# Optimization experiments

Measured on AMD Instinct MI355X. Metric: run time of the kernel, lower is better.

## Reference

```python
import jax, jax.numpy as jnp
import numpy as np

N_SRC, N_DST = 20000, 20000
N = N_SRC + N_DST            # homogeneous node count
E = 320000                   # bipartite edges
H, D, IN = 8, 16, 128        # heads, per-head dim, input dim
TEM = 0.7
NEG_SLOPE = 0.2              # DGL GATConv leaky_relu slope
E_NEG = E - int(round(E * 0.01))  # drop-edge keeps 316800 edges


def setup_inputs() -> dict:
    key = jax.random.key(0)
    ks = jax.random.split(key, 6)
    feat = jax.random.normal(ks[0], (N, IN), jnp.float32)
    edge_src = jax.random.randint(ks[1], (E,), 0, N_SRC, dtype=jnp.int32)
    edge_dst = jax.random.randint(ks[2], (E,), 0, N_DST, dtype=jnp.int32) + N_SRC
    rng = np.random.default_rng(0)
    neg_idx = jnp.asarray(np.sort(rng.permutation(E)[:E_NEG]).astype(np.int32))
    fc_w = jax.random.normal(ks[3], (IN, H * D), jnp.float32) / np.sqrt(IN).astype(np.float32)
    attn_l = jax.random.normal(ks[4], (H, D), jnp.float32) * 0.1
    attn_r = jax.random.normal(ks[5], (H, D), jnp.float32) * 0.1
    bias = jnp.zeros((H * D,), jnp.float32)
    prelu_a = jnp.full((1,), 0.25, jnp.float32)
    return dict(feat=feat, fc_w=fc_w, attn_l=attn_l, attn_r=attn_r, bias=bias,
                prelu_a=prelu_a, edge_src=edge_src, edge_dst=edge_dst, neg_idx=neg_idx)


def _gat(feat, fc_w, attn_l, attn_r, bias, prelu_a, src, dst):
    """DGL GATConv (attn_drop=0, bias=True, activation=PReLU) + self-loops, then head-mean."""
    loop = jnp.arange(N, dtype=src.dtype)
    src = jnp.concatenate([src, loop])
    dst = jnp.concatenate([dst, loop])
    z = (feat @ fc_w).reshape(N, H, D)                 # [N,H,D]
    el = jnp.sum(z * attn_l[None], axis=-1)            # [N,H]
    er = jnp.sum(z * attn_r[None], axis=-1)            # [N,H]
    e = el[src] + er[dst]                              # [E',H]
    e = jnp.where(e >= 0, e, NEG_SLOPE * e)            # leaky_relu
    # segment (edge) softmax over incoming edges of each dst node
    m = jax.ops.segment_max(e, dst, num_segments=N)
    w = jnp.exp(e - m[dst])
    denom = jax.ops.segment_sum(w, dst, num_segments=N)
    alpha = w / denom[dst]                             # [E',H]
    msg = alpha[:, :, None] * z[src]                   # [E',H,D]
    rst = jax.ops.segment_sum(msg, dst, num_segments=N)  # [N,H,D]
    rst = rst + bias.reshape(1, H, D)
    rst = jnp.where(rst >= 0, rst, prelu_a[0] * rst)   # PReLU (single param)
    return jnp.mean(rst, axis=1)                       # [N,D] head-mean


def reference(feat, fc_w, attn_l, attn_r, bias, prelu_a, edge_src, edge_dst, neg_idx):
    h = _gat(feat, fc_w, attn_l, attn_r, bias, prelu_a, edge_src, edge_dst)
    h_neg_full = _gat(feat, fc_w, attn_l, attn_r, bias, prelu_a,
                      edge_src[neg_idx], edge_dst[neg_idx])
    # predict-type (dst) nodes are ids [N_SRC, N)
    h_pos = h[N_SRC:]
    h_neg = h_neg_full[N_SRC:]
    eps = 1e-8
    num = jnp.sum(h_pos * h_neg, axis=-1)
    na = jnp.maximum(jnp.linalg.norm(h_pos, axis=-1), eps)
    nb = jnp.maximum(jnp.linalg.norm(h_neg, axis=-1), eps)
    cos = num / (na * nb)                              # F.cosine_similarity
    loss = jnp.log(jnp.sum(jnp.exp(cos / TEM)))
    return loss, h_pos
```

## Files before the change

kernel.cpp:

```cpp
#include <hip/hip_runtime.h>

#define NSRC 20000
#define NDST 20000
#define NTOT 40000
#define ETOT 320000
#define ENEG 316800
#define NH 8
#define ND 16
#define NHD 128
#define BSTRIDE 136

typedef __bf16 v8bf __attribute__((ext_vector_type(8)));
typedef float v4f __attribute__((ext_vector_type(4)));


__global__ __launch_bounds__(256) void k_front(const float* __restrict__ A,
                                               const float* __restrict__ B,
                                               const float* __restrict__ attn_l,
                                               const float* __restrict__ attn_r,
                                               const int* __restrict__ edge_dst,
                                               const int* __restrict__ neg_idx,
                                               unsigned short* __restrict__ z,
                                               float* __restrict__ el,
                                               float* __restrict__ er,
                                               int* __restrict__ count,
                                               unsigned char* __restrict__ flag) {
    const int tid = threadIdx.x;
    const int bid = blockIdx.x;
    if (bid >= 625) {
        int t0 = (bid - 625) * 256 + tid;
        for (int i = t0; i < ETOT; i += 32768)
            atomicAdd(&count[edge_dst[i] - NSRC], 1);
        for (int i = t0; i < ENEG; i += 32768) flag[neg_idx[i]] = 1;
        return;
    }
    __shared__ __bf16 Bs[128 * BSTRIDE];
    for (int i = tid; i < 4096; i += 256) {
        float4 v = ((const float4*)B)[i];
        int k = (i * 4) >> 7;
        int n = (i * 4) & 127;
        Bs[(n + 0) * BSTRIDE + k] = (__bf16)v.x;
        Bs[(n + 1) * BSTRIDE + k] = (__bf16)v.y;
        Bs[(n + 2) * BSTRIDE + k] = (__bf16)v.z;
        Bs[(n + 3) * BSTRIDE + k] = (__bf16)v.w;
    }
    __syncthreads();
    const int w = tid >> 6, lane = tid & 63;
    const int ml = lane & 15, q = lane >> 4;
    const int gm = bid * 64 + w * 16 + ml;
    v4f acc[8];
#pragma unroll
    for (int n = 0; n < 8; ++n) acc[n] = (v4f){0.f, 0.f, 0.f, 0.f};
#pragma unroll
    for (int ks = 0; ks < 4; ++ks) {
        const int k0 = ks * 32 + q * 8;
        float4 f0 = *(const float4*)(A + (size_t)gm * 128 + k0);
        float4 f1 = *(const float4*)(A + (size_t)gm * 128 + k0 + 4);
        v8bf av;
        av[0] = (__bf16)f0.x; av[1] = (__bf16)f0.y;
        av[2] = (__bf16)f0.z; av[3] = (__bf16)f0.w;
        av[4] = (__bf16)f1.x; av[5] = (__bf16)f1.y;
        av[6] = (__bf16)f1.z; av[7] = (__bf16)f1.w;
#pragma unroll
        for (int n = 0; n < 8; ++n) {
            v8bf bv = *(const v8bf*)(&Bs[(n * 16 + ml) * BSTRIDE + k0]);
            acc[n] = __builtin_amdgcn_mfma_f32_16x16x32_bf16(av, bv, acc[n], 0, 0, 0);
        }
    }
    const int rowbase = bid * 64 + w * 16 + q * 4;
#pragma unroll
    for (int n = 0; n < 8; ++n) {
        float alv = attn_l[n * 16 + ml];
        float arv = attn_r[n * 16 + ml];
#pragma unroll
        for (int r = 0; r < 4; ++r) {
            float v = acc[n][r];
            unsigned int u = __float_as_uint(v);
            unsigned int b = (u + 0x7fffu + ((u >> 16) & 1u)) >> 16;
            z[(size_t)(rowbase + r) * NHD + n * 16 + ml] = (unsigned short)b;
            float pl = v * alv, pr = v * arv;
#pragma unroll
            for (int s = 1; s <= 8; s <<= 1) {
                pl += __shfl_xor(pl, s, 64);
                pr += __shfl_xor(pr, s, 64);
            }
            if (ml == 0) {
                el[(rowbase + r) * NH + n] = pl;
                er[(rowbase + r) * NH + n] = pr;
            }
        }
    }
}

__global__ __launch_bounds__(1024) void k_scan(const int* __restrict__ count,
                                               int* __restrict__ rowstart) {
    __shared__ int wsum[16];
    const int tid = threadIdx.x;
    const int lane = tid & 63, w = tid >> 6;
    const int base = tid * 20;
    int c[20];
    int s = 0;
#pragma unroll
    for (int k = 0; k < 20; ++k) {
        int i = base + k;
        int v = (i < NDST) ? count[i] : 0;
        c[k] = s;
        s += v;
    }
    int v = s;
    for (int sh = 1; sh < 64; sh <<= 1) {
        int t = __shfl_up(v, sh, 64);
        if (lane >= sh) v += t;
    }
    if (lane == 63) wsum[w] = v;
    __syncthreads();
    int carry = 0;
    for (int ww = 0; ww < w; ++ww) carry += wsum[ww];
    int excl = carry + v - s;
#pragma unroll
    for (int k = 0; k < 20; ++k) {
        int i = base + k;
        if (i < NDST) rowstart[i] = excl + c[k];
    }
    if (tid == 1023) rowstart[NDST] = carry + v;
}

__global__ __launch_bounds__(256) void k_scatter(const int* __restrict__ edge_src,
                                                 const int* __restrict__ edge_dst,
                                                 const unsigned char* __restrict__ flag,
                                                 const int* __restrict__ rowstart,
                                                 int* __restrict__ cursor,
                                                 int* __restrict__ csr) {
    int i = blockIdx.x * 256 + threadIdx.x;
    if (i >= ETOT) return;
    int d = edge_dst[i] - NSRC;
    int pos = rowstart[d] + atomicAdd(&cursor[d], 1);
    int v = edge_src[i];
    if (flag[i]) v |= (int)0x80000000u;
    csr[pos] = v;
}

__global__ __launch_bounds__(256) void k_agg(const int* __restrict__ rowstart,
                                             const int* __restrict__ csr,
                                             const unsigned short* __restrict__ z,
                                             const float* __restrict__ el,
                                             const float* __restrict__ er,
                                             const float* __restrict__ bias,
                                             const float* __restrict__ prelu_a,
                                             float* __restrict__ out,
                                             float* __restrict__ expcos) {
    const int lane = threadIdx.x & 63;
    const int wid = threadIdx.x >> 6;
    const int d = (blockIdx.x << 2) + wid;

    const int g = NSRC + d;
    const int hl = lane >> 3;
    const int j8 = lane & 7;
    const float erd = er[g * NH + hl];
    const float aslope = prelu_a[0];
    const float NEGINF = -__builtin_inff();

    float mF = NEGINF, lF = 0.f, mN = NEGINF, lN = 0.f;
    float aF0 = 0.f, aF1 = 0.f, aN0 = 0.f, aN1 = 0.f;
    const int rs = rowstart[d];
    const int deg = rowstart[d + 1] - rs;

    for (int base = 0; base < deg; base += 16) {
        const int j0 = base + j8, j1 = base + 8 + j8;
        int ent0 = (j0 < deg) ? csr[rs + j0] : g;
        int ent1 = (j1 < deg) ? csr[rs + j1] : g;
        unsigned int zr[16];
#pragma unroll
        for (int jj = 0; jj < 16; ++jj) {
            int entry = __shfl((jj < 8) ? ent0 : ent1, jj & 7, 64);
            zr[jj] = *(const unsigned int*)(z + ((size_t)(entry & 0x7FFFFFFF) << 7) + 2 * lane);
        }
        float e0 = el[(size_t)(ent0 & 0x7FFFFFFF) * NH + hl] + erd;
        float e1 = el[(size_t)(ent1 & 0x7FFFFFFF) * NH + hl] + erd;
        e0 = (e0 >= 0.f) ? e0 : 0.2f * e0;
        e1 = (e1 >= 0.f) ? e1 : 0.2f * e1;
        float ev0 = (j0 < deg) ? e0 : NEGINF;
        float ev1 = (j1 < deg) ? e1 : NEGINF;
        const int fl0 = (j0 < deg) && (ent0 < 0);
        const int fl1 = (j1 < deg) && (ent1 < 0);
        float cmF = fmaxf(ev0, ev1);
        float cmN = fmaxf(fl0 ? ev0 : NEGINF, fl1 ? ev1 : NEGINF);
#pragma unroll
        for (int s = 1; s <= 4; s <<= 1) {
            cmF = fmaxf(cmF, __shfl_xor(cmF, s, 64));
            cmN = fmaxf(cmN, __shfl_xor(cmN, s, 64));
        }
        float nmF = fmaxf(mF, cmF);
        float scF = (nmF == mF) ? 1.f : __expf(mF - nmF);
        mF = nmF;
        float nmN = fmaxf(mN, cmN);
        float scN = (nmN == mN) ? 1.f : __expf(mN - nmN);
        mN = nmN;
        float wf0 = __expf(ev0 - mF);
        float wf1 = __expf(ev1 - mF);
        float wn0 = fl0 ? __expf(ev0 - mN) : 0.f;
        float wn1 = fl1 ? __expf(ev1 - mN) : 0.f;
        lF = lF * scF + wf0 + wf1;
        lN = lN * scN + wn0 + wn1;
        float w0 = fl0 ? -wf0 : wf0;
        float w1 = fl1 ? -wf1 : wf1;
        float sNh = __expf(mF - mN);
        aF0 *= scF; aF1 *= scF; aN0 *= scN; aN1 *= scN;
#pragma unroll
        for (int jj = 0; jj < 16; ++jj) {
            float v = __shfl((jj < 8) ? w0 : w1, (lane & 56) | (jj & 7), 64);
            float wf = fabsf(v);
            float wn = (v < 0.f) ? wf * sNh : 0.f;
            float zx = __uint_as_float(zr[jj] << 16);
            float zy = __uint_as_float(zr[jj] & 0xffff0000u);
            aF0 = fmaf(wf, zx, aF0);
            aF1 = fmaf(wf, zy, aF1);
            aN0 = fmaf(wn, zx, aN0);
            aN1 = fmaf(wn, zy, aN1);
        }
    }

    {
        float e = el[g * NH + hl] + erd;
        e = (e >= 0.f) ? e : 0.2f * e;
        float nmF = fmaxf(mF, e);
        float scF = (nmF == mF) ? 1.f : __expf(mF - nmF);
        lF *= scF; aF0 *= scF; aF1 *= scF; mF = nmF;
        float wf = __expf(e - mF);
        float nmN = fmaxf(mN, e);
        float scN = (nmN == mN) ? 1.f : __expf(mN - nmN);
        lN *= scN; aN0 *= scN; aN1 *= scN; mN = nmN;
        float wn = __expf(e - mN);
        if (j8 == 0) { lF += wf; lN += wn; }
        unsigned int zv = *(const unsigned int*)(z + ((size_t)g << 7) + 2 * lane);
        float zx = __uint_as_float(zv << 16);
        float zy = __uint_as_float(zv & 0xffff0000u);
        aF0 = fmaf(wf, zx, aF0);
        aF1 = fmaf(wf, zy, aF1);
        aN0 = fmaf(wn, zx, aN0);
        aN1 = fmaf(wn, zy, aN1);
    }

#pragma unroll
    for (int s = 1; s <= 4; s <<= 1) {
        lF += __shfl_xor(lF, s, 64);
        lN += __shfl_xor(lN, s, 64);
    }
    const int c0 = 2 * lane;
    float b0 = bias[c0], b1 = bias[c0 + 1];
    float rF0 = aF0 / lF + b0, rF1 = aF1 / lF + b1;
    float rN0 = aN0 / lN + b0, rN1 = aN1 / lN + b1;
    rF0 = (rF0 >= 0.f) ? rF0 : aslope * rF0;
    rF1 = (rF1 >= 0.f) ? rF1 : aslope * rF1;
    rN0 = (rN0 >= 0.f) ? rN0 : aslope * rN0;
    rN1 = (rN1 >= 0.f) ? rN1 : aslope * rN1;
#pragma unroll
    for (int s = 8; s <= 32; s <<= 1) {
        rF0 += __shfl_xor(rF0, s, 64);
        rF1 += __shfl_xor(rF1, s, 64);
        rN0 += __shfl_xor(rN0, s, 64);
        rN1 += __shfl_xor(rN1, s, 64);
    }
    float hF0 = rF0 * 0.125f, hF1 = rF1 * 0.125f;
    float hN0 = rN0 * 0.125f, hN1 = rN1 * 0.125f;
    if (lane < 8) {
        out[1 + d * ND + 2 * lane] = hF0;
        out[1 + d * ND + 2 * lane + 1] = hF1;
    }
    float num = hF0 * hN0 + hF1 * hN1;
    float na = hF0 * hF0 + hF1 * hF1;
    float nb = hN0 * hN0 + hN1 * hN1;
#pragma unroll
    for (int s = 1; s <= 4; s <<= 1) {
        num += __shfl_xor(num, s, 64);
        na += __shfl_xor(na, s, 64);
        nb += __shfl_xor(nb, s, 64);
    }
    if (lane == 0) {
        float cosv = num / (fmaxf(sqrtf(na), 1e-8f) * fmaxf(sqrtf(nb), 1e-8f));
        expcos[d] = __expf(cosv / 0.7f);
    }
}

__global__ __launch_bounds__(1024) void k_loss(const float* __restrict__ expcos,
                                               float* __restrict__ out) {
    __shared__ float sbuf[16];
    float s = 0.f;
    for (int i = threadIdx.x; i < NDST; i += 1024) s += expcos[i];
    for (int sh = 1; sh < 64; sh <<= 1) s += __shfl_xor(s, sh, 64);
    if ((threadIdx.x & 63) == 0) sbuf[threadIdx.x >> 6] = s;
    __syncthreads();
    if (threadIdx.x < 16) {
        float t = sbuf[threadIdx.x];
        for (int sh = 1; sh < 16; sh <<= 1) t += __shfl_xor(t, sh, 16);
        if (threadIdx.x == 0) out[0] = logf(t);
    }
}

extern "C" void kernel_launch(void* const* d_in, const int* in_sizes, int n_in,
                              void* d_out, int out_size, void* d_ws, size_t ws_size,
                              hipStream_t stream) {
    const float* feat = (const float*)d_in[0];
    const float* fc_w = (const float*)d_in[1];
    const float* attn_l = (const float*)d_in[2];
    const float* attn_r = (const float*)d_in[3];
    const float* bias = (const float*)d_in[4];
    const float* prelu_a = (const float*)d_in[5];
    const int* edge_src = (const int*)d_in[6];
    const int* edge_dst = (const int*)d_in[7];
    const int* neg_idx = (const int*)d_in[8];
    float* out = (float*)d_out;

    char* ws = (char*)d_ws;
    int* count = (int*)(ws + 0);
    int* cursor = (int*)(ws + 80000);
    unsigned char* flag = (unsigned char*)(ws + 160000);
    int* rowstart = (int*)(ws + 480000);
    int* csr = (int*)(ws + 560064);
    float* expcos = (float*)(ws + 1840064);
    unsigned short* z = (unsigned short*)(ws + 1920064);
    float* el = (float*)(ws + 12160064);
    float* er = (float*)(ws + 13440064);

    hipMemsetAsync(d_ws, 0, 480000, stream);
    k_front<<<753, 256, 0, stream>>>(feat, fc_w, attn_l, attn_r, edge_dst,
                                     neg_idx, z, el, er, count, flag);
    k_scan<<<1, 1024, 0, stream>>>(count, rowstart);
    k_scatter<<<(ETOT + 255) / 256, 256, 0, stream>>>(edge_src, edge_dst, flag,
                                                      rowstart, cursor, csr);
    k_agg<<<NDST / 4, 256, 0, stream>>>(rowstart, csr, z, el, er, bias, prelu_a,
                                        out, expcos);
    k_loss<<<1, 1024, 0, stream>>>(expcos, out);
}
```

Baseline: 178.7 us.

## Replace count/scan CSR with fixed-capacity per-node buckets and share softmax max

```diff
diff --git a/kernel.cpp b/kernel.cpp
--- a/kernel.cpp
+++ b/kernel.cpp
@@ -8,6 +8,7 @@
 #define NH 8
 #define ND 16
 #define NHD 128
+#define BCAP 64
 #define BSTRIDE 136
 
 typedef __bf16 v8bf __attribute__((ext_vector_type(8)));
@@ -18,19 +19,15 @@
                                                const float* __restrict__ B,
                                                const float* __restrict__ attn_l,
                                                const float* __restrict__ attn_r,
-                                               const int* __restrict__ edge_dst,
                                                const int* __restrict__ neg_idx,
                                                unsigned short* __restrict__ z,
                                                float* __restrict__ el,
                                                float* __restrict__ er,
-                                               int* __restrict__ count,
                                                unsigned char* __restrict__ flag) {
     const int tid = threadIdx.x;
     const int bid = blockIdx.x;
     if (bid >= 625) {
         int t0 = (bid - 625) * 256 + tid;
-        for (int i = t0; i < ETOT; i += 32768)
-            atomicAdd(&count[edge_dst[i] - NSRC], 1);
         for (int i = t0; i < ENEG; i += 32768) flag[neg_idx[i]] = 1;
         return;
     }
@@ -92,55 +89,21 @@
     }
 }
 
-__global__ __launch_bounds__(1024) void k_scan(const int* __restrict__ count,
-                                               int* __restrict__ rowstart) {
-    __shared__ int wsum[16];
-    const int tid = threadIdx.x;
-    const int lane = tid & 63, w = tid >> 6;
-    const int base = tid * 20;
-    int c[20];
-    int s = 0;
-#pragma unroll
-    for (int k = 0; k < 20; ++k) {
-        int i = base + k;
-        int v = (i < NDST) ? count[i] : 0;
-        c[k] = s;
-        s += v;
-    }
-    int v = s;
-    for (int sh = 1; sh < 64; sh <<= 1) {
-        int t = __shfl_up(v, sh, 64);
-        if (lane >= sh) v += t;
-    }
-    if (lane == 63) wsum[w] = v;
-    __syncthreads();
-    int carry = 0;
-    for (int ww = 0; ww < w; ++ww) carry += wsum[ww];
-    int excl = carry + v - s;
-#pragma unroll
-    for (int k = 0; k < 20; ++k) {
-        int i = base + k;
-        if (i < NDST) rowstart[i] = excl + c[k];
-    }
-    if (tid == 1023) rowstart[NDST] = carry + v;
-}
-
 __global__ __launch_bounds__(256) void k_scatter(const int* __restrict__ edge_src,
                                                  const int* __restrict__ edge_dst,
                                                  const unsigned char* __restrict__ flag,
-                                                 const int* __restrict__ rowstart,
                                                  int* __restrict__ cursor,
                                                  int* __restrict__ csr) {
     int i = blockIdx.x * 256 + threadIdx.x;
     if (i >= ETOT) return;
     int d = edge_dst[i] - NSRC;
-    int pos = rowstart[d] + atomicAdd(&cursor[d], 1);
+    int slot = atomicAdd(&cursor[d], 1);
     int v = edge_src[i];
     if (flag[i]) v |= (int)0x80000000u;
-    csr[pos] = v;
-}
-
-__global__ __launch_bounds__(256) void k_agg(const int* __restrict__ rowstart,
+    if (slot < BCAP) csr[d * BCAP + slot] = v;
+}
+
+__global__ __launch_bounds__(256) void k_agg(const int* __restrict__ degarr,
                                              const int* __restrict__ csr,
                                              const unsigned short* __restrict__ z,
                                              const float* __restrict__ el,
@@ -156,14 +119,14 @@
     const int g = NSRC + d;
     const int hl = lane >> 3;
     const int j8 = lane & 7;
+    const int rs = d * BCAP;
+    const int deg = degarr[d];
     const float erd = er[g * NH + hl];
     const float aslope = prelu_a[0];
     const float NEGINF = -__builtin_inff();
 
-    float mF = NEGINF, lF = 0.f, mN = NEGINF, lN = 0.f;
+    float mF = NEGINF, lF = 0.f, lN = 0.f;
     float aF0 = 0.f, aF1 = 0.f, aN0 = 0.f, aN1 = 0.f;
-    const int rs = rowstart[d];
-    const int deg = rowstart[d + 1] - rs;
 
     for (int base = 0; base < deg; base += 16) {
         const int j0 = base + j8, j1 = base + 8 + j8;
@@ -183,34 +146,24 @@
         float ev1 = (j1 < deg) ? e1 : NEGINF;
         const int fl0 = (j0 < deg) && (ent0 < 0);
         const int fl1 = (j1 < deg) && (ent1 < 0);
-        float cmF = fmaxf(ev0, ev1);
-        float cmN = fmaxf(fl0 ? ev0 : NEGINF, fl1 ? ev1 : NEGINF);
-#pragma unroll
-        for (int s = 1; s <= 4; s <<= 1) {
-            cmF = fmaxf(cmF, __shfl_xor(cmF, s, 64));
-            cmN = fmaxf(cmN, __shfl_xor(cmN, s, 64));
-        }
-        float nmF = fmaxf(mF, cmF);
-        float scF = (nmF == mF) ? 1.f : __expf(mF - nmF);
-        mF = nmF;
-        float nmN = fmaxf(mN, cmN);
-        float scN = (nmN == mN) ? 1.f : __expf(mN - nmN);
-        mN = nmN;
+        float cm = fmaxf(ev0, ev1);
+#pragma unroll
+        for (int s = 1; s <= 4; s <<= 1) cm = fmaxf(cm, __shfl_xor(cm, s, 64));
+        float nm = fmaxf(mF, cm);
+        float sc = (nm == mF) ? 1.f : __expf(mF - nm);
+        mF = nm;
         float wf0 = __expf(ev0 - mF);
         float wf1 = __expf(ev1 - mF);
-        float wn0 = fl0 ? __expf(ev0 - mN) : 0.f;
-        float wn1 = fl1 ? __expf(ev1 - mN) : 0.f;
-        lF = lF * scF + wf0 + wf1;
-        lN = lN * scN + wn0 + wn1;
+        lF = lF * sc + wf0 + wf1;
+        lN = lN * sc + (fl0 ? wf0 : 0.f) + (fl1 ? wf1 : 0.f);
         float w0 = fl0 ? -wf0 : wf0;
         float w1 = fl1 ? -wf1 : wf1;
-        float sNh = __expf(mF - mN);
-        aF0 *= scF; aF1 *= scF; aN0 *= scN; aN1 *= scN;
+        aF0 *= sc; aF1 *= sc; aN0 *= sc; aN1 *= sc;
 #pragma unroll
         for (int jj = 0; jj < 16; ++jj) {
             float v = __shfl((jj < 8) ? w0 : w1, (lane & 56) | (jj & 7), 64);
             float wf = fabsf(v);
-            float wn = (v < 0.f) ? wf * sNh : 0.f;
+            float wn = (v < 0.f) ? wf : 0.f;
             float zx = __uint_as_float(zr[jj] << 16);
             float zy = __uint_as_float(zr[jj] & 0xffff0000u);
             aF0 = fmaf(wf, zx, aF0);
@@ -223,22 +176,20 @@
     {
         float e = el[g * NH + hl] + erd;
         e = (e >= 0.f) ? e : 0.2f * e;
-        float nmF = fmaxf(mF, e);
-        float scF = (nmF == mF) ? 1.f : __expf(mF - nmF);
-        lF *= scF; aF0 *= scF; aF1 *= scF; mF = nmF;
+        float nm = fmaxf(mF, e);
+        float sc = (nm == mF) ? 1.f : __expf(mF - nm);
+        lF *= sc; lN *= sc;
+        aF0 *= sc; aF1 *= sc; aN0 *= sc; aN1 *= sc;
+        mF = nm;
         float wf = __expf(e - mF);
-        float nmN = fmaxf(mN, e);
-        float scN = (nmN == mN) ? 1.f : __expf(mN - nmN);
-        lN *= scN; aN0 *= scN; aN1 *= scN; mN = nmN;
-        float wn = __expf(e - mN);
-        if (j8 == 0) { lF += wf; lN += wn; }
+        if (j8 == 0) { lF += wf; lN += wf; }
         unsigned int zv = *(const unsigned int*)(z + ((size_t)g << 7) + 2 * lane);
         float zx = __uint_as_float(zv << 16);
         float zy = __uint_as_float(zv & 0xffff0000u);
         aF0 = fmaf(wf, zx, aF0);
         aF1 = fmaf(wf, zy, aF1);
-        aN0 = fmaf(wn, zx, aN0);
-        aN1 = fmaf(wn, zy, aN1);
+        aN0 = fmaf(wf, zx, aN0);
+        aN1 = fmaf(wf, zy, aN1);
     }
 
 #pragma unroll
@@ -312,23 +263,20 @@
     float* out = (float*)d_out;
 
     char* ws = (char*)d_ws;
-    int* count = (int*)(ws + 0);
-    int* cursor = (int*)(ws + 80000);
-    unsigned char* flag = (unsigned char*)(ws + 160000);
-    int* rowstart = (int*)(ws + 480000);
-    int* csr = (int*)(ws + 560064);
-    float* expcos = (float*)(ws + 1840064);
-    unsigned short* z = (unsigned short*)(ws + 1920064);
-    float* el = (float*)(ws + 12160064);
-    float* er = (float*)(ws + 13440064);
-
-    hipMemsetAsync(d_ws, 0, 480000, stream);
-    k_front<<<753, 256, 0, stream>>>(feat, fc_w, attn_l, attn_r, edge_dst,
-                                     neg_idx, z, el, er, count, flag);
-    k_scan<<<1, 1024, 0, stream>>>(count, rowstart);
+    int* cursor = (int*)(ws + 0);
+    unsigned char* flag = (unsigned char*)(ws + 80000);
+    int* csr = (int*)(ws + 400000);
+    float* expcos = (float*)(ws + 5520000);
+    unsigned short* z = (unsigned short*)(ws + 5600000);
+    float* el = (float*)(ws + 15840000);
+    float* er = (float*)(ws + 17120000);
+
+    hipMemsetAsync(d_ws, 0, 400000, stream);
+    k_front<<<753, 256, 0, stream>>>(feat, fc_w, attn_l, attn_r, neg_idx,
+                                     z, el, er, flag);
     k_scatter<<<(ETOT + 255) / 256, 256, 0, stream>>>(edge_src, edge_dst, flag,
-                                                      rowstart, cursor, csr);
-    k_agg<<<NDST / 4, 256, 0, stream>>>(rowstart, csr, z, el, er, bias, prelu_a,
+                                                      cursor, csr);
+    k_agg<<<NDST / 4, 256, 0, stream>>>(cursor, csr, z, el, er, bias, prelu_a,
                                         out, expcos);
     k_loss<<<1, 1024, 0, stream>>>(expcos, out);
 }
```

New measurement: 157.5 us. 1.13x faster.
